# Optimization experiments

Measured on AMD Instinct MI355X. Metric: run time of the kernel, lower is better.

The kernel has to match this reference:

```python
import jax, jax.numpy as jnp
import numpy as np

N = 32          # objects in the (single) image
P = N * (N - 1) # relation pairs
D = 256         # self.dim
M = 14          # mask_size / pooler resolution
OC = 151        # obj classes
RC = 51         # rel classes
RED = D // 4    # attention gate reduction


def setup_inputs() -> dict:
    key = jax.random.key(0)
    ks = jax.random.split(key, 32)
    # all ordered pairs i != j
    ii, jj = np.meshgrid(np.arange(N), np.arange(N), indexing='ij')
    keep = ii != jj
    rel_pair_idxs = jnp.asarray(np.stack([ii[keep], jj[keep]], 1), jnp.int32)  # [P,2]
    # valid xyxy boxes in an 800x600 image
    x1 = jax.random.uniform(ks[0], (N,)) * 600.0
    y1 = jax.random.uniform(ks[1], (N,)) * 400.0
    w = jax.random.uniform(ks[2], (N,)) * 180.0 + 20.0
    h = jax.random.uniform(ks[3], (N,)) * 180.0 + 20.0
    bboxes = jnp.stack([x1, y1, x1 + w, y1 + h], 1).astype(jnp.float32)
    roi_features = jax.random.normal(ks[4], (N, 4096), jnp.float32)
    predict_logits = jax.random.normal(ks[5], (N, OC), jnp.float32)
    union_features = jax.random.normal(ks[6], (P, D, M, M), jnp.float32)
    s = 0.02
    p = dict(
        roi_features=roi_features, bboxes=bboxes, predict_logits=predict_logits,
        union_features=union_features, rel_pair_idxs=rel_pair_idxs,
        W_emb1=jax.random.normal(ks[7], (4096 + OC + 4, D)) * s, b_emb1=jnp.zeros((D,)),
        W_emb2=jax.random.normal(ks[8], (D, D)) * s, b_emb2=jnp.zeros((D,)),
        # stacked SE-attention gates: 0=sbj, 1=obj, 2=bg
        att_fc1_w=jax.random.normal(ks[9], (3, D, RED)) * s, att_fc1_b=jnp.zeros((3, RED)),
        att_fc2_w=jax.random.normal(ks[10], (3, RED, D)) * s, att_fc2_b=jnp.zeros((3, D)),
        W_c1=jax.random.normal(ks[11], (3 * D, D)) * s, b_c1=jnp.zeros((D,)),
        W_c2=jax.random.normal(ks[12], (D, D)) * s, b_c2=jnp.zeros((D,)),
        W_gcn=jax.random.normal(ks[13], (D, D)) * s, b_gcn=jnp.zeros((D,)),
        W_objp=jax.random.normal(ks[14], (D, OC)) * s, b_objp=jnp.zeros((OC,)),
        W_relp=jax.random.normal(ks[15], (D, RC)) * s, b_relp=jnp.zeros((RC,)),
    )
    return p


def _rect_masks(x0, y0, x1, y1):
    # mask[p, r, c] = 1 iff x0<=r<x1 and y0<=c<y1  (matches torch slice write)
    r = jnp.arange(M, dtype=jnp.float32)
    rm = (r[None, :] >= x0[:, None]) & (r[None, :] < x1[:, None])  # [P,M]
    cm = (r[None, :] >= y0[:, None]) & (r[None, :] < y1[:, None])  # [P,M]
    return (rm[:, :, None] & cm[:, None, :]).astype(jnp.float32)   # [P,M,M]


def _masking(union_features, bboxes, pairs):
    sb = bboxes[pairs[:, 0]]  # [P,4]
    ob = bboxes[pairs[:, 1]]
    ux1 = jnp.minimum(sb[:, 0], ob[:, 0])
    uy1 = jnp.minimum(sb[:, 1], ob[:, 1])
    x = jnp.stack([sb[:, 0], sb[:, 2], ob[:, 0], ob[:, 2]], 1) - ux1[:, None]
    y = jnp.stack([sb[:, 1], sb[:, 3], ob[:, 1], ob[:, 3]], 1) - uy1[:, None]
    xr = M / jnp.maximum(x[:, 1], x[:, 3])
    yr = M / jnp.maximum(y[:, 1], y[:, 3])
    xp = jnp.round(x * xr[:, None])
    yp = jnp.round(y * yr[:, None])
    sm = _rect_masks(xp[:, 0], yp[:, 0], xp[:, 1], yp[:, 1])[:, None]  # [P,1,M,M]
    om = _rect_masks(xp[:, 2], yp[:, 2], xp[:, 3], yp[:, 3])[:, None]
    bm = jnp.clip(1.0 - sm - om, 0.0, 1.0)
    return union_features * sm, union_features * om, union_features * bm


def _att_gate(x, w1, b1, w2, b2):
    # SE-style channel attention gate
    s = x.mean((2, 3))                                        # [P,D]
    g = jax.nn.sigmoid(jax.nn.relu(s @ w1 + b1) @ w2 + b2)    # [P,D]
    return x * g[:, :, None, None]


def _adjacency(pairs):
    o2o = jnp.zeros((N, N)).at[pairs[:, 0], pairs[:, 1]].set(1.0)
    ar = jnp.arange(P)
    o2r = jnp.zeros((N, P)).at[pairs[:, 0], ar].set(1.0).at[pairs[:, 1], ar].set(1.0)
    top = jnp.concatenate([o2o, o2r], 1)                     # [N, N+P]
    bot = jnp.concatenate([o2r.T, jnp.zeros((P, P))], 1)     # [P, N+P]
    adj = jnp.concatenate([top, bot], 0)
    return adj + jnp.eye(N + P)


def reference(roi_features, bboxes, predict_logits, union_features, rel_pair_idxs,
              W_emb1, b_emb1, W_emb2, b_emb2,
              att_fc1_w, att_fc1_b, att_fc2_w, att_fc2_b,
              W_c1, b_c1, W_c2, b_c2, W_gcn, b_gcn,
              W_objp, b_objp, W_relp, b_relp):
    pairs = rel_pair_idxs
    # object embedding
    obj_in = jnp.concatenate([roi_features, predict_logits, bboxes], 1)  # [N,4251]
    obj_feats = jax.nn.relu(obj_in @ W_emb1 + b_emb1) @ W_emb2 + b_emb2  # [N,D]
    # masking + attention gates + global avg pool
    sbj, obj, bg = _masking(union_features, bboxes, pairs)
    sbj = _att_gate(sbj, att_fc1_w[0], att_fc1_b[0], att_fc2_w[0], att_fc2_b[0]).mean((2, 3))
    obj = _att_gate(obj, att_fc1_w[1], att_fc1_b[1], att_fc2_w[1], att_fc2_b[1]).mean((2, 3))
    bg = _att_gate(bg, att_fc1_w[2], att_fc1_b[2], att_fc2_w[2], att_fc2_b[2]).mean((2, 3))
    # relational embedding (compose)
    rel = jnp.concatenate([sbj, obj, bg], 1)                 # [P,3D]
    rel_feats = jax.nn.relu(rel @ W_c1 + b_c1) @ W_c2 + b_c2  # [P,D]
    # GCN over object+relation graph (row-normalized adjacency, residual)
    adj = _adjacency(pairs)
    feats = jnp.concatenate([obj_feats, rel_feats], 0)        # [N+P,D]
    norm_adj = adj / adj.sum(1, keepdims=True)
    gcn_out = jax.nn.relu(norm_adj @ (feats @ W_gcn) + b_gcn) + feats
    obj_dists = gcn_out[:N] @ W_objp + b_objp                 # [N,OC]
    rel_dists = gcn_out[N:] @ W_relp + b_relp                 # [P,RC]
    return obj_dists, rel_dists
```

## Files before the change

kernel.cpp:

```cpp
#include <hip/hip_runtime.h>
#include <cstdint>
#include <cstddef>

#define NOBJ 32
#define NP   992
#define DD   256
#define SP   196
#define OC   151
#define RC   51
#define RED  64
#define KIN  4251
#define CH   128
#define KPC  34

#define OFF_PART   0u
#define OFF_OBJF   1048576u
#define OFF_SALL   1056768u
#define OFF_RELF   1818624u
#define OFF_H      2072576u
#define OFF_W2T    2334720u
#define OFF_WC1T   2400256u
#define OFF_WC2T   2596864u
#define OFF_WGT    2662400u
#define OFF_FC1WT  2727936u
#define OFF_FC2WT  2777088u
#define OFF_WOPT   2826240u
#define OFF_WRPT   2864896u

__global__ void k_transpose(const float* __restrict__ W2,  const float* __restrict__ Wc1,
                            const float* __restrict__ Wc2, const float* __restrict__ Wg,
                            const float* __restrict__ f1w, const float* __restrict__ f2w,
                            const float* __restrict__ Wop, const float* __restrict__ Wrp,
                            float* __restrict__ W2T,  float* __restrict__ Wc1T,
                            float* __restrict__ Wc2T, float* __restrict__ WgT,
                            float* __restrict__ f1wT, float* __restrict__ f2wT,
                            float* __restrict__ WopT, float* __restrict__ WrpT) {
  const int b = blockIdx.x, t = threadIdx.x;
  if (b < 256) {
    int idx = b * 256 + t; int k = idx >> 8, c = idx & 255;
    W2T[c * 256 + k] = W2[idx];
  } else if (b < 1024) {
    int idx = (b - 256) * 256 + t; int k = idx >> 8, c = idx & 255;
    Wc1T[c * 768 + k] = Wc1[idx];
  } else if (b < 1280) {
    int idx = (b - 1024) * 256 + t; int k = idx >> 8, c = idx & 255;
    Wc2T[c * 256 + k] = Wc2[idx];
  } else if (b < 1536) {
    int idx = (b - 1280) * 256 + t; int k = idx >> 8, c = idx & 255;
    WgT[c * 256 + k] = Wg[idx];
  } else if (b < 1728) {
    int idx = (b - 1536) * 256 + t; int br = idx >> 14; int rem = idx & 16383;
    int k = rem >> 6, c = rem & 63;
    f1wT[br * 16384 + c * 256 + k] = f1w[idx];
  } else if (b < 1920) {
    int idx = (b - 1728) * 256 + t; int br = idx >> 14; int rem = idx & 16383;
    int k = rem >> 8, c = rem & 255;
    f2wT[br * 16384 + c * 64 + k] = f2w[idx];
  } else if (b < 2071) {
    int idx = (b - 1920) * 256 + t; int k = idx / OC, c = idx - k * OC;
    WopT[c * 256 + k] = Wop[idx];
  } else {
    int idx = (b - 2071) * 256 + t; int k = idx / RC, c = idx - k * RC;
    WrpT[c * 256 + k] = Wrp[idx];
  }
}

__global__ void k_emb1_partial(const float* __restrict__ roi,
                               const float* __restrict__ logits,
                               const float* __restrict__ bbox,
                               const float* __restrict__ W1,
                               float* __restrict__ part) {
  const int chunk = blockIdx.x;
  const int t = threadIdx.x;
  int k0 = chunk * KPC;
  int k1 = k0 + KPC; if (k1 > KIN) k1 = KIN;
  float acc[NOBJ];
#pragma unroll
  for (int i = 0; i < NOBJ; ++i) acc[i] = 0.f;
#pragma unroll 2
  for (int k = k0; k < k1; ++k) {
    float w = W1[(size_t)k * DD + t];
    const float* xp; int stride;
    if (k < 4096)            { xp = roi    + k;               stride = 4096; }
    else if (k < 4096 + OC)  { xp = logits + (k - 4096);      stride = OC;   }
    else                     { xp = bbox   + (k - 4096 - OC); stride = 4;    }
#pragma unroll
    for (int i = 0; i < NOBJ; ++i) { acc[i] += xp[0] * w; xp += stride; }
  }
  float* pout = part + (size_t)chunk * (NOBJ * DD) + t;
#pragma unroll
  for (int i = 0; i < NOBJ; ++i) pout[i * DD] = acc[i];
}

__global__ void k_emb2(const float* __restrict__ part,
                       const float* __restrict__ b1,
                       const float* __restrict__ W2T,
                       const float* __restrict__ b2,
                       float* __restrict__ objf) {
  const int i = blockIdx.x, t = threadIdx.x;
  __shared__ __align__(16) float h[DD];
  float s[8];
#pragma unroll
  for (int u = 0; u < 8; ++u) s[u] = 0.f;
#pragma unroll
  for (int c0 = 0; c0 < CH; c0 += 8) {
#pragma unroll
    for (int u = 0; u < 8; ++u)
      s[u] += part[(size_t)(c0 + u) * (NOBJ * DD) + i * DD + t];
  }
  float tot = ((s[0] + s[1]) + (s[2] + s[3])) + ((s[4] + s[5]) + (s[6] + s[7]));
  h[t] = fmaxf(tot + b1[t], 0.f);
  __syncthreads();
  const float4* w4 = (const float4*)(W2T + (size_t)t * DD);
  float a0 = 0, a1 = 0, a2 = 0, a3 = 0;
#pragma unroll 8
  for (int j = 0; j < DD / 4; ++j) {
    float4 wv = w4[j];
    float4 hv = *(const float4*)&h[4 * j];
    a0 += hv.x * wv.x; a1 += hv.y * wv.y; a2 += hv.z * wv.z; a3 += hv.w * wv.w;
  }
  objf[i * DD + t] = (a0 + a1) + (a2 + a3) + b2[t];
}

__global__ void k_union(const float* __restrict__ uf,
                        const float* __restrict__ bbox,
                        const int* __restrict__ pairs,
                        float* __restrict__ sAll) {
  const int p = blockIdx.x, t = threadIdx.x;
  __shared__ __align__(16) float wS[SP];
  __shared__ __align__(16) float wO[SP];
  __shared__ __align__(16) float wB[SP];
  if (t < SP) {
    int si = pairs[2 * p], oi = pairs[2 * p + 1];
    float sx1 = bbox[si * 4 + 0], sy1 = bbox[si * 4 + 1];
    float sx2 = bbox[si * 4 + 2], sy2 = bbox[si * 4 + 3];
    float ox1 = bbox[oi * 4 + 0], oy1 = bbox[oi * 4 + 1];
    float ox2 = bbox[oi * 4 + 2], oy2 = bbox[oi * 4 + 3];
    float ux = fminf(sx1, ox1), uy = fminf(sy1, oy1);
    float xr = 14.f / fmaxf(sx2 - ux, ox2 - ux);
    float yr = 14.f / fmaxf(sy2 - uy, oy2 - uy);
    float xs0 = rintf((sx1 - ux) * xr), xs1 = rintf((sx2 - ux) * xr);
    float xo0 = rintf((ox1 - ux) * xr), xo1 = rintf((ox2 - ux) * xr);
    float ys0 = rintf((sy1 - uy) * yr), ys1 = rintf((sy2 - uy) * yr);
    float yo0 = rintf((oy1 - uy) * yr), yo1 = rintf((oy2 - uy) * yr);
    int a = t / 14, b = t - a * 14;
    float fa = (float)a, fb = (float)b;
    float sm = (fa >= xs0 && fa < xs1 && fb >= ys0 && fb < ys1) ? 1.f : 0.f;
    float om = (fa >= xo0 && fa < xo1 && fb >= yo0 && fb < yo1) ? 1.f : 0.f;
    float bm = fminf(fmaxf(1.f - sm - om, 0.f), 1.f);
    wS[t] = sm; wO[t] = om; wB[t] = bm;
  }
  __syncthreads();
  const float4* u4 = (const float4*)(uf + ((size_t)p * DD + t) * SP);
  float as0 = 0, as1 = 0, ao0 = 0, ao1 = 0, ab0 = 0, ab1 = 0;
#pragma unroll 7
  for (int j = 0; j < SP / 4; ++j) {
    float4 v  = u4[j];
    float4 ms = *(const float4*)&wS[4 * j];
    float4 mo = *(const float4*)&wO[4 * j];
    float4 mb = *(const float4*)&wB[4 * j];
    as0 += v.x * ms.x + v.y * ms.y;  as1 += v.z * ms.z + v.w * ms.w;
    ao0 += v.x * mo.x + v.y * mo.y;  ao1 += v.z * mo.z + v.w * mo.w;
    ab0 += v.x * mb.x + v.y * mb.y;  ab1 += v.z * mb.z + v.w * mb.w;
  }
  const float inv = 1.f / 196.f;
  float* o = sAll + (size_t)p * 768;
  o[t]       = (as0 + as1) * inv;
  o[256 + t] = (ao0 + ao1) * inv;
  o[512 + t] = (ab0 + ab1) * inv;
}

__global__ void k_attrel(const float* __restrict__ sAll,
                         const float* __restrict__ f1wT, const float* __restrict__ f1b,
                         const float* __restrict__ f2wT, const float* __restrict__ f2b,
                         const float* __restrict__ Wc1T, const float* __restrict__ bc1,
                         const float* __restrict__ Wc2T, const float* __restrict__ bc2,
                         float* __restrict__ relf) {
  const int p0 = blockIdx.x * 4;
  const int t = threadIdx.x;
  __shared__ __align__(16) float sg[4][768];
  __shared__ __align__(16) float ha[4][192];
  __shared__ __align__(16) float h2[4][256];
  {
    const float4* src = (const float4*)(sAll + (size_t)p0 * 768);
    float4* dst = (float4*)&sg[0][0];
#pragma unroll
    for (int j = t; j < 768; j += 256) dst[j] = src[j];
  }
  __syncthreads();
  if (t < 192) {
    const int br = t >> 6, c = t & 63;
    const float4* w4 = (const float4*)(f1wT + (br * 64 + c) * 256);
    const int sb = br * 256;
    float a0 = 0, a1 = 0, a2 = 0, a3 = 0;
#pragma unroll 8
    for (int j = 0; j < 64; ++j) {
      float4 wv = w4[j];
      float4 s0 = *(const float4*)&sg[0][sb + 4 * j];
      float4 s1 = *(const float4*)&sg[1][sb + 4 * j];
      float4 s2 = *(const float4*)&sg[2][sb + 4 * j];
      float4 s3 = *(const float4*)&sg[3][sb + 4 * j];
      a0 += s0.x * wv.x + s0.y * wv.y + s0.z * wv.z + s0.w * wv.w;
      a1 += s1.x * wv.x + s1.y * wv.y + s1.z * wv.z + s1.w * wv.w;
      a2 += s2.x * wv.x + s2.y * wv.y + s2.z * wv.z + s2.w * wv.w;
      a3 += s3.x * wv.x + s3.y * wv.y + s3.z * wv.z + s3.w * wv.w;
    }
    float bb = f1b[br * 64 + c];
    ha[0][t] = fmaxf(a0 + bb, 0.f);
    ha[1][t] = fmaxf(a1 + bb, 0.f);
    ha[2][t] = fmaxf(a2 + bb, 0.f);
    ha[3][t] = fmaxf(a3 + bb, 0.f);
  }
  __syncthreads();
#pragma unroll
  for (int br = 0; br < 3; ++br) {
    const float4* w4 = (const float4*)(f2wT + br * 16384 + t * 64);
    const int hb = br * 64;
    float a0 = 0, a1 = 0, a2 = 0, a3 = 0;
#pragma unroll
    for (int j = 0; j < 16; ++j) {
      float4 wv = w4[j];
      float4 v0 = *(const float4*)&ha[0][hb + 4 * j];
      float4 v1 = *(const float4*)&ha[1][hb + 4 * j];
      float4 v2 = *(const float4*)&ha[2][hb + 4 * j];
      float4 v3 = *(const float4*)&ha[3][hb + 4 * j];
      a0 += v0.x * wv.x + v0.y * wv.y + v0.z * wv.z + v0.w * wv.w;
      a1 += v1.x * wv.x + v1.y * wv.y + v1.z * wv.z + v1.w * wv.w;
      a2 += v2.x * wv.x + v2.y * wv.y + v2.z * wv.z + v2.w * wv.w;
      a3 += v3.x * wv.x + v3.y * wv.y + v3.z * wv.z + v3.w * wv.w;
    }
    float bb = f2b[br * 256 + t];
    int ci = br * 256 + t;
    sg[0][ci] *= 1.f / (1.f + expf(-(a0 + bb)));
    sg[1][ci] *= 1.f / (1.f + expf(-(a1 + bb)));
    sg[2][ci] *= 1.f / (1.f + expf(-(a2 + bb)));
    sg[3][ci] *= 1.f / (1.f + expf(-(a3 + bb)));
  }
  __syncthreads();
  {
    const float4* w4 = (const float4*)(Wc1T + (size_t)t * 768);
    float a0 = 0, a1 = 0, a2 = 0, a3 = 0;
#pragma unroll 8
    for (int j = 0; j < 192; ++j) {
      float4 wv = w4[j];
      float4 g0 = *(const float4*)&sg[0][4 * j];
      float4 g1 = *(const float4*)&sg[1][4 * j];
      float4 g2 = *(const float4*)&sg[2][4 * j];
      float4 g3 = *(const float4*)&sg[3][4 * j];
      a0 += g0.x * wv.x + g0.y * wv.y + g0.z * wv.z + g0.w * wv.w;
      a1 += g1.x * wv.x + g1.y * wv.y + g1.z * wv.z + g1.w * wv.w;
      a2 += g2.x * wv.x + g2.y * wv.y + g2.z * wv.z + g2.w * wv.w;
      a3 += g3.x * wv.x + g3.y * wv.y + g3.z * wv.z + g3.w * wv.w;
    }
    float bb = bc1[t];
    h2[0][t] = fmaxf(a0 + bb, 0.f);
    h2[1][t] = fmaxf(a1 + bb, 0.f);
    h2[2][t] = fmaxf(a2 + bb, 0.f);
    h2[3][t] = fmaxf(a3 + bb, 0.f);
  }
  __syncthreads();
  {
    const float4* w4 = (const float4*)(Wc2T + (size_t)t * 256);
    float a0 = 0, a1 = 0, a2 = 0, a3 = 0;
#pragma unroll 8
    for (int j = 0; j < 64; ++j) {
      float4 wv = w4[j];
      float4 v0 = *(const float4*)&h2[0][4 * j];
      float4 v1 = *(const float4*)&h2[1][4 * j];
      float4 v2 = *(const float4*)&h2[2][4 * j];
      float4 v3 = *(const float4*)&h2[3][4 * j];
      a0 += v0.x * wv.x + v0.y * wv.y + v0.z * wv.z + v0.w * wv.w;
      a1 += v1.x * wv.x + v1.y * wv.y + v1.z * wv.z + v1.w * wv.w;
      a2 += v2.x * wv.x + v2.y * wv.y + v2.z * wv.z + v2.w * wv.w;
      a3 += v3.x * wv.x + v3.y * wv.y + v3.z * wv.z + v3.w * wv.w;
    }
    float bb = bc2[t];
    relf[(size_t)(p0 + 0) * DD + t] = a0 + bb;
    relf[(size_t)(p0 + 1) * DD + t] = a1 + bb;
    relf[(size_t)(p0 + 2) * DD + t] = a2 + bb;
    relf[(size_t)(p0 + 3) * DD + t] = a3 + bb;
  }
}

__global__ void k_gcn_h(const float* __restrict__ objf, const float* __restrict__ relf,
                        const float* __restrict__ WgT, float* __restrict__ H) {
  const int r0 = blockIdx.x * 2;
  const int t = threadIdx.x;
  __shared__ __align__(16) float fin[2][DD];
#pragma unroll
  for (int r = 0; r < 2; ++r) {
    int row = r0 + r;
    fin[r][t] = (row < NOBJ) ? objf[row * DD + t]
                             : relf[(size_t)(row - NOBJ) * DD + t];
  }
  __syncthreads();
  const float4* w4 = (const float4*)(WgT + (size_t)t * DD);
  float a0 = 0, a1 = 0;
#pragma unroll 8
  for (int j = 0; j < DD / 4; ++j) {
    float4 wv = w4[j];
    float4 f0 = *(const float4*)&fin[0][4 * j];
    float4 f1 = *(const float4*)&fin[1][4 * j];
    a0 += f0.x * wv.x + f0.y * wv.y + f0.z * wv.z + f0.w * wv.w;
    a1 += f1.x * wv.x + f1.y * wv.y + f1.z * wv.z + f1.w * wv.w;
  }
  H[(size_t)(r0 + 0) * DD + t] = a0;
  H[(size_t)(r0 + 1) * DD + t] = a1;
}

__global__ void k_obj_out(const float* __restrict__ H, const float* __restrict__ objf,
                          const int* __restrict__ pairs, const float* __restrict__ bg,
                          const float* __restrict__ WopT, const float* __restrict__ bop,
                          float* __restrict__ out) {
  const int i = blockIdx.x, t = threadIdx.x;
  const int slice = t >> 8, tt = t & 255;
  __shared__ int2 pr[NP];
  __shared__ float red[4][DD];
  __shared__ __align__(16) float gr[DD];
  const int2* p2 = (const int2*)pairs;
  for (int r = t; r < NP; r += 1024) pr[r] = p2[r];
  __syncthreads();
  float acc = 0.f;
  if (slice == 0) {
#pragma unroll 8
    for (int j = 0; j < NOBJ; ++j) acc += H[j * DD + tt];
  }
  const int rbeg = slice * 248;
#pragma unroll 8
  for (int r = rbeg; r < rbeg + 248; ++r) {
    int2 q = pr[r];
    float v = H[(size_t)(NOBJ + r) * DD + tt];
    if (q.x == i || q.y == i) acc += v;
  }
  red[slice][tt] = acc;
  __syncthreads();
  if (t < DD) {
    float pre = (red[0][t] + red[1][t] + red[2][t] + red[3][t]) * (1.f / 94.f);
    gr[t] = fmaxf(pre + bg[t], 0.f) + objf[i * DD + t];
  }
  __syncthreads();
  float hsum = 0.f;
  if (tt < OC) {
    const float4* w4 = (const float4*)(WopT + tt * 256 + slice * 64);
#pragma unroll
    for (int j = 0; j < 16; ++j) {
      float4 wv = w4[j];
      float4 gv = *(const float4*)&gr[slice * 64 + 4 * j];
      hsum += gv.x * wv.x + gv.y * wv.y + gv.z * wv.z + gv.w * wv.w;
    }
  }
  red[slice][tt] = hsum;
  __syncthreads();
  if (t < OC)
    out[i * OC + t] = red[0][t] + red[1][t] + red[2][t] + red[3][t] + bop[t];
}

__global__ void k_rel_out(const float* __restrict__ H, const float* __restrict__ relf,
                          const int* __restrict__ pairs, const float* __restrict__ bg,
                          const float* __restrict__ WrpT, const float* __restrict__ brp,
                          float* __restrict__ out) {
  const int r = blockIdx.x, t = threadIdx.x;
  __shared__ __align__(16) float gr[DD];
  __shared__ float red[4][64];
  int si = pairs[2 * r], oi = pairs[2 * r + 1];
  float hsum = H[si * DD + t] + H[oi * DD + t] + H[(size_t)(NOBJ + r) * DD + t];
  gr[t] = fmaxf(hsum * (1.f / 3.f) + bg[t], 0.f) + relf[(size_t)r * DD + t];
  __syncthreads();
  const int q = t >> 6, c = t & 63;
  float a = 0.f;
  if (c < RC) {
    const float4* w4 = (const float4*)(WrpT + c * 256 + q * 64);
#pragma unroll
    for (int j = 0; j < 16; ++j) {
      float4 wv = w4[j];
      float4 gv = *(const float4*)&gr[q * 64 + 4 * j];
      a += gv.x * wv.x + gv.y * wv.y + gv.z * wv.z + gv.w * wv.w;
    }
  }
  red[q][c] = a;
  __syncthreads();
  if (t < RC)
    out[NOBJ * OC + (size_t)r * RC + t] =
        red[0][t] + red[1][t] + red[2][t] + red[3][t] + brp[t];
}

extern "C" void kernel_launch(void* const* d_in, const int* in_sizes, int n_in,
                              void* d_out, int out_size, void* d_ws, size_t ws_size,
                              hipStream_t stream) {
  const float* roi   = (const float*)d_in[0];
  const float* bbox  = (const float*)d_in[1];
  const float* logit = (const float*)d_in[2];
  const float* uf    = (const float*)d_in[3];
  const int*   pairs = (const int*)d_in[4];
  const float* W1    = (const float*)d_in[5];
  const float* b1    = (const float*)d_in[6];
  const float* W2    = (const float*)d_in[7];
  const float* b2    = (const float*)d_in[8];
  const float* fc1w  = (const float*)d_in[9];
  const float* fc1b  = (const float*)d_in[10];
  const float* fc2w  = (const float*)d_in[11];
  const float* fc2b  = (const float*)d_in[12];
  const float* Wc1   = (const float*)d_in[13];
  const float* bc1   = (const float*)d_in[14];
  const float* Wc2   = (const float*)d_in[15];
  const float* bc2   = (const float*)d_in[16];
  const float* Wg    = (const float*)d_in[17];
  const float* bg    = (const float*)d_in[18];
  const float* Wop   = (const float*)d_in[19];
  const float* bop   = (const float*)d_in[20];
  const float* Wrp   = (const float*)d_in[21];
  const float* brp   = (const float*)d_in[22];

  float* ws    = (float*)d_ws;
  float* part  = ws + OFF_PART;
  float* objf  = ws + OFF_OBJF;
  float* sAll  = ws + OFF_SALL;
  float* relf  = ws + OFF_RELF;
  float* Hbuf  = ws + OFF_H;
  float* W2T   = ws + OFF_W2T;
  float* Wc1T  = ws + OFF_WC1T;
  float* Wc2T  = ws + OFF_WC2T;
  float* WgT   = ws + OFF_WGT;
  float* f1wT  = ws + OFF_FC1WT;
  float* f2wT  = ws + OFF_FC2WT;
  float* WopT  = ws + OFF_WOPT;
  float* WrpT  = ws + OFF_WRPT;
  float* out   = (float*)d_out;

  k_transpose<<<2122, 256, 0, stream>>>(W2, Wc1, Wc2, Wg, fc1w, fc2w, Wop, Wrp,
                                        W2T, Wc1T, Wc2T, WgT, f1wT, f2wT, WopT, WrpT);
  k_emb1_partial<<<CH, 256, 0, stream>>>(roi, logit, bbox, W1, part);
  k_union<<<NP, 256, 0, stream>>>(uf, bbox, pairs, sAll);
  k_emb2<<<NOBJ, 256, 0, stream>>>(part, b1, W2T, b2, objf);
  k_attrel<<<NP / 4, 256, 0, stream>>>(sAll, f1wT, fc1b, f2wT, fc2b,
                                       Wc1T, bc1, Wc2T, bc2, relf);
  k_gcn_h<<<(NOBJ + NP) / 2, 256, 0, stream>>>(objf, relf, WgT, Hbuf);
  k_obj_out<<<NOBJ, 1024, 0, stream>>>(Hbuf, objf, pairs, bg, WopT, bop, out);
  k_rel_out<<<NP, 256, 0, stream>>>(Hbuf, relf, pairs, bg, WrpT, brp, out);
}
```

Baseline: 541.5 us.

## Merge independent stages into fewer launches via block-index dispatch

Cuts the pipeline from eight launches to four. The weight transposes, emb1 partial sums and the union masking/pooling now share one grid, dispatched by block index. The attention/relation MLP is merged with emb2, and the two output heads share another grid. The transpose now uses a grid-stride loop with coalesced writes and gathered reads. The attrel stage changes from 256 threads each handling 4 pairs to 1024 threads handling one pair per 256-thread group, which loses weight reuse across pairs in registers and may raise L2 traffic.

```diff
diff --git a/kernel.cpp b/kernel.cpp
--- a/kernel.cpp
+++ b/kernel.cpp
@@ -27,258 +27,208 @@
 #define OFF_WOPT   2826240u
 #define OFF_WRPT   2864896u
 
-__global__ void k_transpose(const float* __restrict__ W2,  const float* __restrict__ Wc1,
-                            const float* __restrict__ Wc2, const float* __restrict__ Wg,
-                            const float* __restrict__ f1w, const float* __restrict__ f2w,
-                            const float* __restrict__ Wop, const float* __restrict__ Wrp,
-                            float* __restrict__ W2T,  float* __restrict__ Wc1T,
-                            float* __restrict__ Wc2T, float* __restrict__ WgT,
-                            float* __restrict__ f1wT, float* __restrict__ f2wT,
-                            float* __restrict__ WopT, float* __restrict__ WrpT) {
+#define TR_TOT 543232
+
+__global__ void k_pre(const float* __restrict__ uf,
+                      const float* __restrict__ bbox,
+                      const int* __restrict__ pairs,
+                      const float* __restrict__ roi,
+                      const float* __restrict__ logits,
+                      const float* __restrict__ W1,
+                      const float* __restrict__ W2,  const float* __restrict__ Wc1,
+                      const float* __restrict__ Wc2, const float* __restrict__ Wg,
+                      const float* __restrict__ f1w, const float* __restrict__ f2w,
+                      const float* __restrict__ Wop, const float* __restrict__ Wrp,
+                      float* __restrict__ sAll, float* __restrict__ part,
+                      float* __restrict__ W2T,  float* __restrict__ Wc1T,
+                      float* __restrict__ Wc2T, float* __restrict__ WgT,
+                      float* __restrict__ f1wT, float* __restrict__ f2wT,
+                      float* __restrict__ WopT, float* __restrict__ WrpT) {
   const int b = blockIdx.x, t = threadIdx.x;
-  if (b < 256) {
-    int idx = b * 256 + t; int k = idx >> 8, c = idx & 255;
-    W2T[c * 256 + k] = W2[idx];
-  } else if (b < 1024) {
-    int idx = (b - 256) * 256 + t; int k = idx >> 8, c = idx & 255;
-    Wc1T[c * 768 + k] = Wc1[idx];
-  } else if (b < 1280) {
-    int idx = (b - 1024) * 256 + t; int k = idx >> 8, c = idx & 255;
-    Wc2T[c * 256 + k] = Wc2[idx];
-  } else if (b < 1536) {
-    int idx = (b - 1280) * 256 + t; int k = idx >> 8, c = idx & 255;
-    WgT[c * 256 + k] = Wg[idx];
-  } else if (b < 1728) {
-    int idx = (b - 1536) * 256 + t; int br = idx >> 14; int rem = idx & 16383;
-    int k = rem >> 6, c = rem & 63;
-    f1wT[br * 16384 + c * 256 + k] = f1w[idx];
-  } else if (b < 1920) {
-    int idx = (b - 1728) * 256 + t; int br = idx >> 14; int rem = idx & 16383;
-    int k = rem >> 8, c = rem & 255;
-    f2wT[br * 16384 + c * 64 + k] = f2w[idx];
-  } else if (b < 2071) {
-    int idx = (b - 1920) * 256 + t; int k = idx / OC, c = idx - k * OC;
-    WopT[c * 256 + k] = Wop[idx];
+  if (b < NP) {
+    const int p = b;
+    __shared__ __align__(16) float wS[SP];
+    __shared__ __align__(16) float wO[SP];
+    __shared__ __align__(16) float wB[SP];
+    if (t < SP) {
+      int si = pairs[2 * p], oi = pairs[2 * p + 1];
+      float sx1 = bbox[si * 4 + 0], sy1 = bbox[si * 4 + 1];
+      float sx2 = bbox[si * 4 + 2], sy2 = bbox[si * 4 + 3];
+      float ox1 = bbox[oi * 4 + 0], oy1 = bbox[oi * 4 + 1];
+      float ox2 = bbox[oi * 4 + 2], oy2 = bbox[oi * 4 + 3];
+      float ux = fminf(sx1, ox1), uy = fminf(sy1, oy1);
+      float xr = 14.f / fmaxf(sx2 - ux, ox2 - ux);
+      float yr = 14.f / fmaxf(sy2 - uy, oy2 - uy);
+      float xs0 = rintf((sx1 - ux) * xr), xs1 = rintf((sx2 - ux) * xr);
+      float xo0 = rintf((ox1 - ux) * xr), xo1 = rintf((ox2 - ux) * xr);
+      float ys0 = rintf((sy1 - uy) * yr), ys1 = rintf((sy2 - uy) * yr);
+      float yo0 = rintf((oy1 - uy) * yr), yo1 = rintf((oy2 - uy) * yr);
+      int a = t / 14, bb = t - a * 14;
+      float fa = (float)a, fb = (float)bb;
+      float sm = (fa >= xs0 && fa < xs1 && fb >= ys0 && fb < ys1) ? 1.f : 0.f;
+      float om = (fa >= xo0 && fa < xo1 && fb >= yo0 && fb < yo1) ? 1.f : 0.f;
+      float bm = fminf(fmaxf(1.f - sm - om, 0.f), 1.f);
+      wS[t] = sm; wO[t] = om; wB[t] = bm;
+    }
+    __syncthreads();
+    const float4* u4 = (const float4*)(uf + ((size_t)p * DD + t) * SP);
+    float as0 = 0, as1 = 0, ao0 = 0, ao1 = 0, ab0 = 0, ab1 = 0;
+#pragma unroll 7
+    for (int j = 0; j < SP / 4; ++j) {
+      float4 v  = u4[j];
+      float4 ms = *(const float4*)&wS[4 * j];
+      float4 mo = *(const float4*)&wO[4 * j];
+      float4 mb = *(const float4*)&wB[4 * j];
+      as0 += v.x * ms.x + v.y * ms.y;  as1 += v.z * ms.z + v.w * ms.w;
+      ao0 += v.x * mo.x + v.y * mo.y;  ao1 += v.z * mo.z + v.w * mo.w;
+      ab0 += v.x * mb.x + v.y * mb.y;  ab1 += v.z * mb.z + v.w * mb.w;
+    }
+    const float inv = 1.f / 196.f;
+    float* o = sAll + (size_t)p * 768;
+    o[t]       = (as0 + as1) * inv;
+    o[256 + t] = (ao0 + ao1) * inv;
+    o[512 + t] = (ab0 + ab1) * inv;
+  } else if (b < NP + CH) {
+    const int chunk = b - NP;
+    int k0 = chunk * KPC;
+    int k1 = k0 + KPC; if (k1 > KIN) k1 = KIN;
+    float acc[NOBJ];
+#pragma unroll
+    for (int i = 0; i < NOBJ; ++i) acc[i] = 0.f;
+#pragma unroll 2
+    for (int k = k0; k < k1; ++k) {
+      float w = W1[(size_t)k * DD + t];
+      const float* xp; int stride;
+      if (k < 4096)            { xp = roi    + k;               stride = 4096; }
+      else if (k < 4096 + OC)  { xp = logits + (k - 4096);      stride = OC;   }
+      else                     { xp = bbox   + (k - 4096 - OC); stride = 4;    }
+#pragma unroll
+      for (int i = 0; i < NOBJ; ++i) { acc[i] += xp[0] * w; xp += stride; }
+    }
+    float* pout = part + (size_t)chunk * (NOBJ * DD) + t;
+#pragma unroll
+    for (int i = 0; i < NOBJ; ++i) pout[i * DD] = acc[i];
   } else {
-    int idx = (b - 2071) * 256 + t; int k = idx / RC, c = idx - k * RC;
-    WrpT[c * 256 + k] = Wrp[idx];
-  }
-}
-
-__global__ void k_emb1_partial(const float* __restrict__ roi,
-                               const float* __restrict__ logits,
-                               const float* __restrict__ bbox,
-                               const float* __restrict__ W1,
-                               float* __restrict__ part) {
-  const int chunk = blockIdx.x;
-  const int t = threadIdx.x;
-  int k0 = chunk * KPC;
-  int k1 = k0 + KPC; if (k1 > KIN) k1 = KIN;
-  float acc[NOBJ];
-#pragma unroll
-  for (int i = 0; i < NOBJ; ++i) acc[i] = 0.f;
-#pragma unroll 2
-  for (int k = k0; k < k1; ++k) {
-    float w = W1[(size_t)k * DD + t];
-    const float* xp; int stride;
-    if (k < 4096)            { xp = roi    + k;               stride = 4096; }
-    else if (k < 4096 + OC)  { xp = logits + (k - 4096);      stride = OC;   }
-    else                     { xp = bbox   + (k - 4096 - OC); stride = 4;    }
-#pragma unroll
-    for (int i = 0; i < NOBJ; ++i) { acc[i] += xp[0] * w; xp += stride; }
-  }
-  float* pout = part + (size_t)chunk * (NOBJ * DD) + t;
-#pragma unroll
-  for (int i = 0; i < NOBJ; ++i) pout[i * DD] = acc[i];
-}
-
-__global__ void k_emb2(const float* __restrict__ part,
-                       const float* __restrict__ b1,
-                       const float* __restrict__ W2T,
-                       const float* __restrict__ b2,
-                       float* __restrict__ objf) {
-  const int i = blockIdx.x, t = threadIdx.x;
-  __shared__ __align__(16) float h[DD];
-  float s[8];
-#pragma unroll
-  for (int u = 0; u < 8; ++u) s[u] = 0.f;
-#pragma unroll
-  for (int c0 = 0; c0 < CH; c0 += 8) {
-#pragma unroll
-    for (int u = 0; u < 8; ++u)
-      s[u] += part[(size_t)(c0 + u) * (NOBJ * DD) + i * DD + t];
-  }
-  float tot = ((s[0] + s[1]) + (s[2] + s[3])) + ((s[4] + s[5]) + (s[6] + s[7]));
-  h[t] = fmaxf(tot + b1[t], 0.f);
-  __syncthreads();
-  const float4* w4 = (const float4*)(W2T + (size_t)t * DD);
-  float a0 = 0, a1 = 0, a2 = 0, a3 = 0;
-#pragma unroll 8
-  for (int j = 0; j < DD / 4; ++j) {
-    float4 wv = w4[j];
-    float4 hv = *(const float4*)&h[4 * j];
-    a0 += hv.x * wv.x; a1 += hv.y * wv.y; a2 += hv.z * wv.z; a3 += hv.w * wv.w;
-  }
-  objf[i * DD + t] = (a0 + a1) + (a2 + a3) + b2[t];
-}
-
-__global__ void k_union(const float* __restrict__ uf,
-                        const float* __restrict__ bbox,
-                        const int* __restrict__ pairs,
-                        float* __restrict__ sAll) {
-  const int p = blockIdx.x, t = threadIdx.x;
-  __shared__ __align__(16) float wS[SP];
-  __shared__ __align__(16) float wO[SP];
-  __shared__ __align__(16) float wB[SP];
-  if (t < SP) {
-    int si = pairs[2 * p], oi = pairs[2 * p + 1];
-    float sx1 = bbox[si * 4 + 0], sy1 = bbox[si * 4 + 1];
-    float sx2 = bbox[si * 4 + 2], sy2 = bbox[si * 4 + 3];
-    float ox1 = bbox[oi * 4 + 0], oy1 = bbox[oi * 4 + 1];
-    float ox2 = bbox[oi * 4 + 2], oy2 = bbox[oi * 4 + 3];
-    float ux = fminf(sx1, ox1), uy = fminf(sy1, oy1);
-    float xr = 14.f / fmaxf(sx2 - ux, ox2 - ux);
-    float yr = 14.f / fmaxf(sy2 - uy, oy2 - uy);
-    float xs0 = rintf((sx1 - ux) * xr), xs1 = rintf((sx2 - ux) * xr);
-    float xo0 = rintf((ox1 - ux) * xr), xo1 = rintf((ox2 - ux) * xr);
-    float ys0 = rintf((sy1 - uy) * yr), ys1 = rintf((sy2 - uy) * yr);
-    float yo0 = rintf((oy1 - uy) * yr), yo1 = rintf((oy2 - uy) * yr);
-    int a = t / 14, b = t - a * 14;
-    float fa = (float)a, fb = (float)b;
-    float sm = (fa >= xs0 && fa < xs1 && fb >= ys0 && fb < ys1) ? 1.f : 0.f;
-    float om = (fa >= xo0 && fa < xo1 && fb >= yo0 && fb < yo1) ? 1.f : 0.f;
-    float bm = fminf(fmaxf(1.f - sm - om, 0.f), 1.f);
-    wS[t] = sm; wO[t] = om; wB[t] = bm;
-  }
-  __syncthreads();
-  const float4* u4 = (const float4*)(uf + ((size_t)p * DD + t) * SP);
-  float as0 = 0, as1 = 0, ao0 = 0, ao1 = 0, ab0 = 0, ab1 = 0;
-#pragma unroll 7
-  for (int j = 0; j < SP / 4; ++j) {
-    float4 v  = u4[j];
-    float4 ms = *(const float4*)&wS[4 * j];
-    float4 mo = *(const float4*)&wO[4 * j];
-    float4 mb = *(const float4*)&wB[4 * j];
-    as0 += v.x * ms.x + v.y * ms.y;  as1 += v.z * ms.z + v.w * ms.w;
-    ao0 += v.x * mo.x + v.y * mo.y;  ao1 += v.z * mo.z + v.w * mo.w;
-    ab0 += v.x * mb.x + v.y * mb.y;  ab1 += v.z * mb.z + v.w * mb.w;
-  }
-  const float inv = 1.f / 196.f;
-  float* o = sAll + (size_t)p * 768;
-  o[t]       = (as0 + as1) * inv;
-  o[256 + t] = (ao0 + ao1) * inv;
-  o[512 + t] = (ab0 + ab1) * inv;
-}
-
-__global__ void k_attrel(const float* __restrict__ sAll,
-                         const float* __restrict__ f1wT, const float* __restrict__ f1b,
-                         const float* __restrict__ f2wT, const float* __restrict__ f2b,
-                         const float* __restrict__ Wc1T, const float* __restrict__ bc1,
-                         const float* __restrict__ Wc2T, const float* __restrict__ bc2,
-                         float* __restrict__ relf) {
-  const int p0 = blockIdx.x * 4;
-  const int t = threadIdx.x;
+    for (int o = (b - NP - CH) * 256 + t; o < TR_TOT; o += 256 * 256) {
+      float v; float* dst;
+      if (o < 65536)       { int q = o;          v = W2 [(q & 255) * 256 + (q >> 8)]; dst = W2T  + q; }
+      else if (o < 262144) { int q = o - 65536;  int c = q / 768, k = q - c * 768;
+                             v = Wc1[k * 256 + c];                                    dst = Wc1T + q; }
+      else if (o < 327680) { int q = o - 262144; v = Wc2[(q & 255) * 256 + (q >> 8)]; dst = Wc2T + q; }
+      else if (o < 393216) { int q = o - 327680; v = Wg [(q & 255) * 256 + (q >> 8)]; dst = WgT  + q; }
+      else if (o < 442368) { int q = o - 393216;
+                             v = f1w[(q >> 14) * 16384 + (q & 255) * 64 + ((q >> 8) & 63)];
+                             dst = f1wT + q; }
+      else if (o < 491520) { int q = o - 442368;
+                             v = f2w[(q >> 14) * 16384 + (q & 63) * 256 + ((q >> 6) & 255)];
+                             dst = f2wT + q; }
+      else if (o < 530176) { int q = o - 491520; v = Wop[(q & 255) * OC + (q >> 8)];  dst = WopT + q; }
+      else                 { int q = o - 530176; v = Wrp[(q & 255) * RC + (q >> 8)];  dst = WrpT + q; }
+      *dst = v;
+    }
+  }
+}
+
+__global__ void __launch_bounds__(1024, 1)
+k_mid(const float* __restrict__ sAll,
+      const float* __restrict__ f1wT, const float* __restrict__ f1b,
+      const float* __restrict__ f2wT, const float* __restrict__ f2b,
+      const float* __restrict__ Wc1T, const float* __restrict__ bc1,
+      const float* __restrict__ Wc2T, const float* __restrict__ bc2,
+      const float* __restrict__ part, const float* __restrict__ b1,
+      const float* __restrict__ W2T,  const float* __restrict__ b2,
+      float* __restrict__ relf, float* __restrict__ objf) {
+  const int b = blockIdx.x, t = threadIdx.x;
+  const int p = t >> 8, tt = t & 255;
   __shared__ __align__(16) float sg[4][768];
   __shared__ __align__(16) float ha[4][192];
   __shared__ __align__(16) float h2[4][256];
-  {
-    const float4* src = (const float4*)(sAll + (size_t)p0 * 768);
-    float4* dst = (float4*)&sg[0][0];
-#pragma unroll
-    for (int j = t; j < 768; j += 256) dst[j] = src[j];
-  }
-  __syncthreads();
-  if (t < 192) {
-    const int br = t >> 6, c = t & 63;
-    const float4* w4 = (const float4*)(f1wT + (br * 64 + c) * 256);
-    const int sb = br * 256;
+  if (b < NP / 4) {
+    const int p0 = b * 4;
+    {
+      const float4* src = (const float4*)(sAll + (size_t)p0 * 768);
+      float4* dst = (float4*)&sg[0][0];
+      if (t < 768) dst[t] = src[t];
+    }
+    __syncthreads();
+    if (tt < 192) {
+      const int br = tt >> 6, c = tt & 63;
+      const float4* w4 = (const float4*)(f1wT + (br * 64 + c) * 256);
+      const float* sp = &sg[p][br * 256];
+      float a0 = 0, a1 = 0, a2 = 0, a3 = 0;
+#pragma unroll 8
+      for (int j = 0; j < 64; ++j) {
+        float4 wv = w4[j];
+        float4 sv = *(const float4*)&sp[4 * j];
+        a0 += sv.x * wv.x; a1 += sv.y * wv.y; a2 += sv.z * wv.z; a3 += sv.w * wv.w;
+      }
+      ha[p][tt] = fmaxf((a0 + a1) + (a2 + a3) + f1b[br * 64 + c], 0.f);
+    }
+    __syncthreads();
+#pragma unroll
+    for (int br = 0; br < 3; ++br) {
+      const float4* w4 = (const float4*)(f2wT + br * 16384 + tt * 64);
+      const float* hp = &ha[p][br * 64];
+      float a0 = 0, a1 = 0, a2 = 0, a3 = 0;
+#pragma unroll
+      for (int j = 0; j < 16; ++j) {
+        float4 wv = w4[j];
+        float4 hv = *(const float4*)&hp[4 * j];
+        a0 += hv.x * wv.x; a1 += hv.y * wv.y; a2 += hv.z * wv.z; a3 += hv.w * wv.w;
+      }
+      float g = 1.f / (1.f + expf(-((a0 + a1) + (a2 + a3) + f2b[br * 256 + tt])));
+      sg[p][br * 256 + tt] *= g;
+    }
+    __syncthreads();
+    {
+      const float4* w4 = (const float4*)(Wc1T + (size_t)tt * 768);
+      const float* gp = &sg[p][0];
+      float a0 = 0, a1 = 0, a2 = 0, a3 = 0;
+#pragma unroll 8
+      for (int j = 0; j < 192; ++j) {
+        float4 wv = w4[j];
+        float4 gv = *(const float4*)&gp[4 * j];
+        a0 += gv.x * wv.x; a1 += gv.y * wv.y; a2 += gv.z * wv.z; a3 += gv.w * wv.w;
+      }
+      h2[p][tt] = fmaxf((a0 + a1) + (a2 + a3) + bc1[tt], 0.f);
+    }
+    __syncthreads();
+    {
+      const float4* w4 = (const float4*)(Wc2T + (size_t)tt * 256);
+      const float* hp = &h2[p][0];
+      float a0 = 0, a1 = 0, a2 = 0, a3 = 0;
+#pragma unroll 8
+      for (int j = 0; j < 64; ++j) {
+        float4 wv = w4[j];
+        float4 hv = *(const float4*)&hp[4 * j];
+        a0 += hv.x * wv.x; a1 += hv.y * wv.y; a2 += hv.z * wv.z; a3 += hv.w * wv.w;
+      }
+      relf[(size_t)(p0 + p) * DD + tt] = (a0 + a1) + (a2 + a3) + bc2[tt];
+    }
+  } else {
+    const int r = (b - NP / 4) * 4 + p;
+    float s[8];
+#pragma unroll
+    for (int u = 0; u < 8; ++u) s[u] = 0.f;
+#pragma unroll
+    for (int c0 = 0; c0 < CH; c0 += 8) {
+#pragma unroll
+      for (int u = 0; u < 8; ++u)
+        s[u] += part[(size_t)(c0 + u) * (NOBJ * DD) + r * DD + tt];
+    }
+    float tot = ((s[0] + s[1]) + (s[2] + s[3])) + ((s[4] + s[5]) + (s[6] + s[7]));
+    h2[p][tt] = fmaxf(tot + b1[tt], 0.f);
+    __syncthreads();
+    const float4* w4 = (const float4*)(W2T + (size_t)tt * DD);
+    const float* hp = &h2[p][0];
     float a0 = 0, a1 = 0, a2 = 0, a3 = 0;
 #pragma unroll 8
     for (int j = 0; j < 64; ++j) {
       float4 wv = w4[j];
-      float4 s0 = *(const float4*)&sg[0][sb + 4 * j];
-      float4 s1 = *(const float4*)&sg[1][sb + 4 * j];
-      float4 s2 = *(const float4*)&sg[2][sb + 4 * j];
-      float4 s3 = *(const float4*)&sg[3][sb + 4 * j];
-      a0 += s0.x * wv.x + s0.y * wv.y + s0.z * wv.z + s0.w * wv.w;
-      a1 += s1.x * wv.x + s1.y * wv.y + s1.z * wv.z + s1.w * wv.w;
-      a2 += s2.x * wv.x + s2.y * wv.y + s2.z * wv.z + s2.w * wv.w;
-      a3 += s3.x * wv.x + s3.y * wv.y + s3.z * wv.z + s3.w * wv.w;
-    }
-    float bb = f1b[br * 64 + c];
-    ha[0][t] = fmaxf(a0 + bb, 0.f);
-    ha[1][t] = fmaxf(a1 + bb, 0.f);
-    ha[2][t] = fmaxf(a2 + bb, 0.f);
-    ha[3][t] = fmaxf(a3 + bb, 0.f);
-  }
-  __syncthreads();
-#pragma unroll
-  for (int br = 0; br < 3; ++br) {
-    const float4* w4 = (const float4*)(f2wT + br * 16384 + t * 64);
-    const int hb = br * 64;
-    float a0 = 0, a1 = 0, a2 = 0, a3 = 0;
-#pragma unroll
-    for (int j = 0; j < 16; ++j) {
-      float4 wv = w4[j];
-      float4 v0 = *(const float4*)&ha[0][hb + 4 * j];
-      float4 v1 = *(const float4*)&ha[1][hb + 4 * j];
-      float4 v2 = *(const float4*)&ha[2][hb + 4 * j];
-      float4 v3 = *(const float4*)&ha[3][hb + 4 * j];
-      a0 += v0.x * wv.x + v0.y * wv.y + v0.z * wv.z + v0.w * wv.w;
-      a1 += v1.x * wv.x + v1.y * wv.y + v1.z * wv.z + v1.w * wv.w;
-      a2 += v2.x * wv.x + v2.y * wv.y + v2.z * wv.z + v2.w * wv.w;
-      a3 += v3.x * wv.x + v3.y * wv.y + v3.z * wv.z + v3.w * wv.w;
-    }
-    float bb = f2b[br * 256 + t];
-    int ci = br * 256 + t;
-    sg[0][ci] *= 1.f / (1.f + expf(-(a0 + bb)));
-    sg[1][ci] *= 1.f / (1.f + expf(-(a1 + bb)));
-    sg[2][ci] *= 1.f / (1.f + expf(-(a2 + bb)));
-    sg[3][ci] *= 1.f / (1.f + expf(-(a3 + bb)));
-  }
-  __syncthreads();
-  {
-    const float4* w4 = (const float4*)(Wc1T + (size_t)t * 768);
-    float a0 = 0, a1 = 0, a2 = 0, a3 = 0;
-#pragma unroll 8
-    for (int j = 0; j < 192; ++j) {
-      float4 wv = w4[j];
-      float4 g0 = *(const float4*)&sg[0][4 * j];
-      float4 g1 = *(const float4*)&sg[1][4 * j];
-      float4 g2 = *(const float4*)&sg[2][4 * j];
-      float4 g3 = *(const float4*)&sg[3][4 * j];
-      a0 += g0.x * wv.x + g0.y * wv.y + g0.z * wv.z + g0.w * wv.w;
-      a1 += g1.x * wv.x + g1.y * wv.y + g1.z * wv.z + g1.w * wv.w;
-      a2 += g2.x * wv.x + g2.y * wv.y + g2.z * wv.z + g2.w * wv.w;
-      a3 += g3.x * wv.x + g3.y * wv.y + g3.z * wv.z + g3.w * wv.w;
-    }
-    float bb = bc1[t];
-    h2[0][t] = fmaxf(a0 + bb, 0.f);
-    h2[1][t] = fmaxf(a1 + bb, 0.f);
-    h2[2][t] = fmaxf(a2 + bb, 0.f);
-    h2[3][t] = fmaxf(a3 + bb, 0.f);
-  }
-  __syncthreads();
-  {
-    const float4* w4 = (const float4*)(Wc2T + (size_t)t * 256);
-    float a0 = 0, a1 = 0, a2 = 0, a3 = 0;
-#pragma unroll 8
-    for (int j = 0; j < 64; ++j) {
-      float4 wv = w4[j];
-      float4 v0 = *(const float4*)&h2[0][4 * j];
-      float4 v1 = *(const float4*)&h2[1][4 * j];
-      float4 v2 = *(const float4*)&h2[2][4 * j];
-      float4 v3 = *(const float4*)&h2[3][4 * j];
-      a0 += v0.x * wv.x + v0.y * wv.y + v0.z * wv.z + v0.w * wv.w;
-      a1 += v1.x * wv.x + v1.y * wv.y + v1.z * wv.z + v1.w * wv.w;
-      a2 += v2.x * wv.x + v2.y * wv.y + v2.z * wv.z + v2.w * wv.w;
-      a3 += v3.x * wv.x + v3.y * wv.y + v3.z * wv.z + v3.w * wv.w;
-    }
-    float bb = bc2[t];
-    relf[(size_t)(p0 + 0) * DD + t] = a0 + bb;
-    relf[(size_t)(p0 + 1) * DD + t] = a1 + bb;
-    relf[(size_t)(p0 + 2) * DD + t] = a2 + bb;
-    relf[(size_t)(p0 + 3) * DD + t] = a3 + bb;
+      float4 hv = *(const float4*)&hp[4 * j];
+      a0 += hv.x * wv.x; a1 += hv.y * wv.y; a2 += hv.z * wv.z; a3 += hv.w * wv.w;
+    }
+    objf[r * DD + tt] = (a0 + a1) + (a2 + a3) + b2[tt];
   }
 }
 
@@ -308,80 +258,82 @@
   H[(size_t)(r0 + 1) * DD + t] = a1;
 }
 
-__global__ void k_obj_out(const float* __restrict__ H, const float* __restrict__ objf,
-                          const int* __restrict__ pairs, const float* __restrict__ bg,
-                          const float* __restrict__ WopT, const float* __restrict__ bop,
-                          float* __restrict__ out) {
-  const int i = blockIdx.x, t = threadIdx.x;
-  const int slice = t >> 8, tt = t & 255;
-  __shared__ int2 pr[NP];
-  __shared__ float red[4][DD];
-  __shared__ __align__(16) float gr[DD];
-  const int2* p2 = (const int2*)pairs;
-  for (int r = t; r < NP; r += 1024) pr[r] = p2[r];
-  __syncthreads();
-  float acc = 0.f;
-  if (slice == 0) {
-#pragma unroll 8
-    for (int j = 0; j < NOBJ; ++j) acc += H[j * DD + tt];
-  }
-  const int rbeg = slice * 248;
-#pragma unroll 8
-  for (int r = rbeg; r < rbeg + 248; ++r) {
-    int2 q = pr[r];
-    float v = H[(size_t)(NOBJ + r) * DD + tt];
-    if (q.x == i || q.y == i) acc += v;
-  }
-  red[slice][tt] = acc;
-  __syncthreads();
-  if (t < DD) {
-    float pre = (red[0][t] + red[1][t] + red[2][t] + red[3][t]) * (1.f / 94.f);
-    gr[t] = fmaxf(pre + bg[t], 0.f) + objf[i * DD + t];
-  }
-  __syncthreads();
-  float hsum = 0.f;
-  if (tt < OC) {
-    const float4* w4 = (const float4*)(WopT + tt * 256 + slice * 64);
-#pragma unroll
-    for (int j = 0; j < 16; ++j) {
-      float4 wv = w4[j];
-      float4 gv = *(const float4*)&gr[slice * 64 + 4 * j];
-      hsum += gv.x * wv.x + gv.y * wv.y + gv.z * wv.z + gv.w * wv.w;
-    }
-  }
-  red[slice][tt] = hsum;
-  __syncthreads();
-  if (t < OC)
-    out[i * OC + t] = red[0][t] + red[1][t] + red[2][t] + red[3][t] + bop[t];
-}
-
-__global__ void k_rel_out(const float* __restrict__ H, const float* __restrict__ relf,
-                          const int* __restrict__ pairs, const float* __restrict__ bg,
-                          const float* __restrict__ WrpT, const float* __restrict__ brp,
-                          float* __restrict__ out) {
-  const int r = blockIdx.x, t = threadIdx.x;
-  __shared__ __align__(16) float gr[DD];
-  __shared__ float red[4][64];
-  int si = pairs[2 * r], oi = pairs[2 * r + 1];
-  float hsum = H[si * DD + t] + H[oi * DD + t] + H[(size_t)(NOBJ + r) * DD + t];
-  gr[t] = fmaxf(hsum * (1.f / 3.f) + bg[t], 0.f) + relf[(size_t)r * DD + t];
-  __syncthreads();
-  const int q = t >> 6, c = t & 63;
-  float a = 0.f;
-  if (c < RC) {
-    const float4* w4 = (const float4*)(WrpT + c * 256 + q * 64);
-#pragma unroll
-    for (int j = 0; j < 16; ++j) {
-      float4 wv = w4[j];
-      float4 gv = *(const float4*)&gr[q * 64 + 4 * j];
-      a += gv.x * wv.x + gv.y * wv.y + gv.z * wv.z + gv.w * wv.w;
-    }
-  }
-  red[q][c] = a;
-  __syncthreads();
-  if (t < RC)
-    out[NOBJ * OC + (size_t)r * RC + t] =
-        red[0][t] + red[1][t] + red[2][t] + red[3][t] + brp[t];
+__global__ void __launch_bounds__(1024, 1)
+k_heads(const float* __restrict__ H, const float* __restrict__ objf,
+        const float* __restrict__ relf, const int* __restrict__ pairs,
+        const float* __restrict__ bg,
+        const float* __restrict__ WopT, const float* __restrict__ bop,
+        const float* __restrict__ WrpT, const float* __restrict__ brp,
+        float* __restrict__ out) {
+  const int b = blockIdx.x, t = threadIdx.x;
+  const int p = t >> 8, tt = t & 255;
+  if (b < NP / 4) {
+    __shared__ __align__(16) float gr[4][DD];
+    __shared__ float red[4][4][64];
+    const int r = b * 4 + p;
+    int si = pairs[2 * r], oi = pairs[2 * r + 1];
+    float hsum = H[si * DD + tt] + H[oi * DD + tt] + H[(size_t)(NOBJ + r) * DD + tt];
+    gr[p][tt] = fmaxf(hsum * (1.f / 3.f) + bg[tt], 0.f) + relf[(size_t)r * DD + tt];
+    __syncthreads();
+    const int q = tt >> 6, c = tt & 63;
+    float a = 0.f;
+    if (c < RC) {
+      const float4* w4 = (const float4*)(WrpT + c * 256 + q * 64);
+#pragma unroll
+      for (int j = 0; j < 16; ++j) {
+        float4 wv = w4[j];
+        float4 gv = *(const float4*)&gr[p][q * 64 + 4 * j];
+        a += gv.x * wv.x + gv.y * wv.y + gv.z * wv.z + gv.w * wv.w;
+      }
+    }
+    red[p][q][c] = a;
+    __syncthreads();
+    if (tt < RC)
+      out[NOBJ * OC + (size_t)r * RC + tt] =
+          red[p][0][tt] + red[p][1][tt] + red[p][2][tt] + red[p][3][tt] + brp[tt];
+  } else {
+    const int i = b - NP / 4;
+    const int slice = p;
+    __shared__ int2 pr[NP];
+    __shared__ float red2[4][DD];
+    __shared__ __align__(16) float gro[DD];
+    const int2* p2 = (const int2*)pairs;
+    for (int r = t; r < NP; r += 1024) pr[r] = p2[r];
+    __syncthreads();
+    float acc = 0.f;
+    if (slice == 0) {
+#pragma unroll 8
+      for (int j = 0; j < NOBJ; ++j) acc += H[j * DD + tt];
+    }
+    const int rbeg = slice * 248;
+#pragma unroll 8
+    for (int r = rbeg; r < rbeg + 248; ++r) {
+      int2 q = pr[r];
+      float v = H[(size_t)(NOBJ + r) * DD + tt];
+      if (q.x == i || q.y == i) acc += v;
+    }
+    red2[slice][tt] = acc;
+    __syncthreads();
+    if (t < DD) {
+      float pre = (red2[0][t] + red2[1][t] + red2[2][t] + red2[3][t]) * (1.f / 94.f);
+      gro[t] = fmaxf(pre + bg[t], 0.f) + objf[i * DD + t];
+    }
+    __syncthreads();
+    float hsum = 0.f;
+    if (tt < OC) {
+      const float4* w4 = (const float4*)(WopT + tt * 256 + slice * 64);
+#pragma unroll
+      for (int j = 0; j < 16; ++j) {
+        float4 wv = w4[j];
+        float4 gv = *(const float4*)&gro[slice * 64 + 4 * j];
+        hsum += gv.x * wv.x + gv.y * wv.y + gv.z * wv.z + gv.w * wv.w;
+      }
+    }
+    red2[slice][tt] = hsum;
+    __syncthreads();
+    if (t < OC)
+      out[i * OC + t] = red2[0][t] + red2[1][t] + red2[2][t] + red2[3][t] + bop[t];
+  }
 }
 
 extern "C" void kernel_launch(void* const* d_in, const int* in_sizes, int n_in,
@@ -427,14 +379,14 @@
   float* WrpT  = ws + OFF_WRPT;
   float* out   = (float*)d_out;
 
-  k_transpose<<<2122, 256, 0, stream>>>(W2, Wc1, Wc2, Wg, fc1w, fc2w, Wop, Wrp,
-                                        W2T, Wc1T, Wc2T, WgT, f1wT, f2wT, WopT, WrpT);
-  k_emb1_partial<<<CH, 256, 0, stream>>>(roi, logit, bbox, W1, part);
-  k_union<<<NP, 256, 0, stream>>>(uf, bbox, pairs, sAll);
-  k_emb2<<<NOBJ, 256, 0, stream>>>(part, b1, W2T, b2, objf);
-  k_attrel<<<NP / 4, 256, 0, stream>>>(sAll, f1wT, fc1b, f2wT, fc2b,
-                                       Wc1T, bc1, Wc2T, bc2, relf);
+  k_pre<<<NP + CH + 256, 256, 0, stream>>>(uf, bbox, pairs, roi, logit, W1,
+                                           W2, Wc1, Wc2, Wg, fc1w, fc2w, Wop, Wrp,
+                                           sAll, part, W2T, Wc1T, Wc2T, WgT,
+                                           f1wT, f2wT, WopT, WrpT);
+  k_mid<<<NP / 4 + 8, 1024, 0, stream>>>(sAll, f1wT, fc1b, f2wT, fc2b,
+                                         Wc1T, bc1, Wc2T, bc2,
+                                         part, b1, W2T, b2, relf, objf);
   k_gcn_h<<<(NOBJ + NP) / 2, 256, 0, stream>>>(objf, relf, WgT, Hbuf);
-  k_obj_out<<<NOBJ, 1024, 0, stream>>>(Hbuf, objf, pairs, bg, WopT, bop, out);
-  k_rel_out<<<NP, 256, 0, stream>>>(Hbuf, relf, pairs, bg, WrpT, brp, out);
-}
+  k_heads<<<NP / 4 + NOBJ, 1024, 0, stream>>>(Hbuf, objf, relf, pairs, bg,
+                                              WopT, bop, WrpT, brp, out);
+}
```

Result: slower. 610.6 us (+12.8%).
